# Optimization experiments

Hardware: AMD Instinct MI355X
Metric: run time of the kernel (lower is better)

Reference implementation:

```python
import jax, jax.numpy as jnp
import numpy as np

SEQ = 16384
D = 1024


def setup_inputs() -> dict:
    key = jax.random.key(0)
    k1, k2, k3, k4 = jax.random.split(key, 4)
    return {
        "G_M1": jax.random.normal(k1, (SEQ, D), dtype=jnp.float32),
        "G_M2": jax.random.normal(k2, (SEQ, D), dtype=jnp.float32),
        "wp1": jax.random.normal(k3, (1, D), dtype=jnp.float32),
        "wp2": jax.random.normal(k4, (1, D), dtype=jnp.float32),
    }


def reference(G_M1, G_M2, wp1, wp2):
    # Original: per-row tensordot(wp1, G_M1[i][:, None]) -> [1,1], concat along
    # axis 1 -> p1 of shape [1, SEQ]; same for p2; softmax over the seq axis.
    # This is exactly a single matvec per head followed by softmax.
    p1 = jnp.einsum("od,sd->os", wp1, G_M1)  # [1, SEQ]
    p2 = jnp.einsum("od,sd->os", wp2, G_M2)  # [1, SEQ]
    p1_pred = jax.nn.softmax(p1, axis=-1)
    p2_pred = jax.nn.softmax(p2, axis=-1)
    return (p1_pred, p2_pred)
```

## Files before the change

kernel.cpp:

```cpp
#include <hip/hip_runtime.h>
#include <hip/hip_bf16.h>
#include <math.h>

#define SEQ 16384
#define D   1024
#define NBLK_DOT 2048
#define WAVES_PER_BLK 4

__global__ __launch_bounds__(256) void dot_partial_kernel(
    const float* __restrict__ g1, const float* __restrict__ g2,
    const float* __restrict__ wp1, const float* __restrict__ wp2,
    float* __restrict__ logits,
    float* __restrict__ blk_m, float* __restrict__ blk_s) {
  const int lane = threadIdx.x & 63;
  const int wid  = threadIdx.x >> 6;
  const int w    = blockIdx.x * WAVES_PER_BLK + wid;
  const int r0   = w * 4;
  const bool head1 = (r0 >= SEQ);
  const float* g  = head1 ? g2 : g1;
  const float* wp = head1 ? wp2 : wp1;
  const int row0  = head1 ? (r0 - SEQ) : r0;

  const float4* wpv = (const float4*)wp;
  float4 wv[4];
#pragma unroll
  for (int k = 0; k < 4; ++k) wv[k] = wpv[lane + 64 * k];

  const float4* rv = (const float4*)(g + (size_t)row0 * D);
  float acc0 = 0.f, acc1 = 0.f, acc2 = 0.f, acc3 = 0.f;
#pragma unroll
  for (int k = 0; k < 4; ++k) {
    const int o = lane + 64 * k;
    float4 a0 = rv[o];
    float4 a1 = rv[o + 256];
    float4 a2 = rv[o + 512];
    float4 a3 = rv[o + 768];
    float4 wk = wv[k];
    acc0 = fmaf(a0.x, wk.x, fmaf(a0.y, wk.y, fmaf(a0.z, wk.z, fmaf(a0.w, wk.w, acc0))));
    acc1 = fmaf(a1.x, wk.x, fmaf(a1.y, wk.y, fmaf(a1.z, wk.z, fmaf(a1.w, wk.w, acc1))));
    acc2 = fmaf(a2.x, wk.x, fmaf(a2.y, wk.y, fmaf(a2.z, wk.z, fmaf(a2.w, wk.w, acc2))));
    acc3 = fmaf(a3.x, wk.x, fmaf(a3.y, wk.y, fmaf(a3.z, wk.z, fmaf(a3.w, wk.w, acc3))));
  }
#pragma unroll
  for (int off = 32; off > 0; off >>= 1) {
    acc0 += __shfl_xor(acc0, off, 64);
    acc1 += __shfl_xor(acc1, off, 64);
    acc2 += __shfl_xor(acc2, off, 64);
    acc3 += __shfl_xor(acc3, off, 64);
  }
  if (lane == 0) {
    *(float4*)(logits + r0) = make_float4(acc0, acc1, acc2, acc3);
  }

  float mw = fmaxf(fmaxf(acc0, acc1), fmaxf(acc2, acc3));
  float sw = __expf(acc0 - mw) + __expf(acc1 - mw) +
             __expf(acc2 - mw) + __expf(acc3 - mw);

  __shared__ float lm[WAVES_PER_BLK], ls[WAVES_PER_BLK];
  if (lane == 0) { lm[wid] = mw; ls[wid] = sw; }
  __syncthreads();
  if (threadIdx.x == 0) {
    float M = fmaxf(fmaxf(lm[0], lm[1]), fmaxf(lm[2], lm[3]));
    float S = ls[0] * __expf(lm[0] - M) + ls[1] * __expf(lm[1] - M) +
              ls[2] * __expf(lm[2] - M) + ls[3] * __expf(lm[3] - M);
    blk_m[blockIdx.x] = M;
    blk_s[blockIdx.x] = S;
  }
}

__global__ __launch_bounds__(1024) void stats_kernel(
    const float* __restrict__ blk_m, const float* __restrict__ blk_s,
    float* __restrict__ stats) {
  const int h    = blockIdx.x;
  const int tid  = threadIdx.x;
  const int lane = tid & 63;
  const int wid  = tid >> 6;

  float m = blk_m[h * 1024 + tid];
  float s = blk_s[h * 1024 + tid];

  __shared__ float sm[16], ssum[16];

  float mm = m;
#pragma unroll
  for (int off = 32; off > 0; off >>= 1)
    mm = fmaxf(mm, __shfl_xor(mm, off, 64));
  if (lane == 0) sm[wid] = mm;
  __syncthreads();
  float M = sm[0];
#pragma unroll
  for (int i = 1; i < 16; ++i) M = fmaxf(M, sm[i]);

  float c = s * __expf(m - M);
#pragma unroll
  for (int off = 32; off > 0; off >>= 1)
    c += __shfl_xor(c, off, 64);
  if (lane == 0) ssum[wid] = c;
  __syncthreads();
  if (tid == 0) {
    float S = 0.f;
#pragma unroll
    for (int i = 0; i < 16; ++i) S += ssum[i];
    stats[2 * h]     = M;
    stats[2 * h + 1] = 1.0f / S;
  }
}

__global__ __launch_bounds__(256) void normalize_kernel(
    const float4* __restrict__ logits4, const float* __restrict__ stats,
    float4* __restrict__ out4) {
  const int i = blockIdx.x * blockDim.x + threadIdx.x;
  const int h = i >> 12;
  const float M    = stats[2 * h];
  const float invS = stats[2 * h + 1];
  float4 v = logits4[i];
  float4 o;
  o.x = __expf(v.x - M) * invS;
  o.y = __expf(v.y - M) * invS;
  o.z = __expf(v.z - M) * invS;
  o.w = __expf(v.w - M) * invS;
  out4[i] = o;
}

extern "C" void kernel_launch(void* const* d_in, const int* in_sizes, int n_in,
                              void* d_out, int out_size, void* d_ws, size_t ws_size,
                              hipStream_t stream) {
  const float* g1  = (const float*)d_in[0];
  const float* g2  = (const float*)d_in[1];
  const float* wp1 = (const float*)d_in[2];
  const float* wp2 = (const float*)d_in[3];
  float* out = (float*)d_out;

  float* logits = (float*)d_ws;
  float* blk_m  = logits + 2 * SEQ;
  float* blk_s  = blk_m + NBLK_DOT;
  float* stats  = blk_s + NBLK_DOT;

  dot_partial_kernel<<<NBLK_DOT, 256, 0, stream>>>(g1, g2, wp1, wp2,
                                                   logits, blk_m, blk_s);
  stats_kernel<<<2, 1024, 0, stream>>>(blk_m, blk_s, stats);
  normalize_kernel<<<32, 256, 0, stream>>>((const float4*)logits, stats,
                                           (float4*)out);
}
```

Baseline: 153.3 us.

## Fuse softmax stats into normalize kernel, use nontemporal loads, two rows per wave

Merges the stats and normalize kernels into one finalize kernel, where each block redundantly reduces its head's per-block max/sum, which removes one launch. The dot kernel now handles two rows per wave across twice as many blocks. All row loads are issued up front as nontemporal loads so the streamed inputs do not pollute the cache. The cost is redundant reduction work in each of the 32 finalize blocks and a different load pattern in the bandwidth-bound dot kernel.

```diff
diff --git a/kernel.cpp b/kernel.cpp
--- a/kernel.cpp
+++ b/kernel.cpp
@@ -4,59 +4,71 @@
 
 #define SEQ 16384
 #define D   1024
-#define NBLK_DOT 2048
-#define WAVES_PER_BLK 4
+#define NBLK_DOT 4096
+#define ROWS_PER_WAVE 2
 
-__global__ __launch_bounds__(256) void dot_partial_kernel(
+typedef float floatx4 __attribute__((ext_vector_type(4)));
+
+__device__ __forceinline__ floatx4 nt_load4(const float* p) {
+  return __builtin_nontemporal_load((const floatx4*)p);
+}
+
+__global__ void dot_partial_kernel(
     const float* __restrict__ g1, const float* __restrict__ g2,
     const float* __restrict__ wp1, const float* __restrict__ wp2,
     float* __restrict__ logits,
     float* __restrict__ blk_m, float* __restrict__ blk_s) {
   const int lane = threadIdx.x & 63;
   const int wid  = threadIdx.x >> 6;
-  const int w    = blockIdx.x * WAVES_PER_BLK + wid;
-  const int r0   = w * 4;
-  const bool head1 = (r0 >= SEQ);
+  const int w    = blockIdx.x * 4 + wid;
+  const int r0   = w * ROWS_PER_WAVE;
+  const bool head1 = (blockIdx.x >= NBLK_DOT / 2);
   const float* g  = head1 ? g2 : g1;
   const float* wp = head1 ? wp2 : wp1;
   const int row0  = head1 ? (r0 - SEQ) : r0;
 
-  const float4* wpv = (const float4*)wp;
-  float4 wv[4];
+  floatx4 wv[4];
 #pragma unroll
-  for (int k = 0; k < 4; ++k) wv[k] = wpv[lane + 64 * k];
+  for (int k = 0; k < 4; ++k)
+    wv[k] = *((const floatx4*)wp + lane + 64 * k);
 
-  const float4* rv = (const float4*)(g + (size_t)row0 * D);
-  float acc0 = 0.f, acc1 = 0.f, acc2 = 0.f, acc3 = 0.f;
+  const float* row = g + (size_t)row0 * D;
+
+  floatx4 a0 = nt_load4(row + 4 * (lane));
+  floatx4 a1 = nt_load4(row + 4 * (lane + 64));
+  floatx4 a2 = nt_load4(row + 4 * (lane + 128));
+  floatx4 a3 = nt_load4(row + 4 * (lane + 192));
+  floatx4 b0 = nt_load4(row + D + 4 * (lane));
+  floatx4 b1 = nt_load4(row + D + 4 * (lane + 64));
+  floatx4 b2 = nt_load4(row + D + 4 * (lane + 128));
+  floatx4 b3 = nt_load4(row + D + 4 * (lane + 192));
+
+  float acc0 = 0.f, acc1 = 0.f;
 #pragma unroll
-  for (int k = 0; k < 4; ++k) {
-    const int o = lane + 64 * k;
-    float4 a0 = rv[o];
-    float4 a1 = rv[o + 256];
-    float4 a2 = rv[o + 512];
-    float4 a3 = rv[o + 768];
-    float4 wk = wv[k];
-    acc0 = fmaf(a0.x, wk.x, fmaf(a0.y, wk.y, fmaf(a0.z, wk.z, fmaf(a0.w, wk.w, acc0))));
-    acc1 = fmaf(a1.x, wk.x, fmaf(a1.y, wk.y, fmaf(a1.z, wk.z, fmaf(a1.w, wk.w, acc1))));
-    acc2 = fmaf(a2.x, wk.x, fmaf(a2.y, wk.y, fmaf(a2.z, wk.z, fmaf(a2.w, wk.w, acc2))));
-    acc3 = fmaf(a3.x, wk.x, fmaf(a3.y, wk.y, fmaf(a3.z, wk.z, fmaf(a3.w, wk.w, acc3))));
+  for (int e = 0; e < 4; ++e) {
+    acc0 = fmaf(a0[e], wv[0][e], acc0);
+    acc0 = fmaf(a1[e], wv[1][e], acc0);
+    acc0 = fmaf(a2[e], wv[2][e], acc0);
+    acc0 = fmaf(a3[e], wv[3][e], acc0);
+    acc1 = fmaf(b0[e], wv[0][e], acc1);
+    acc1 = fmaf(b1[e], wv[1][e], acc1);
+    acc1 = fmaf(b2[e], wv[2][e], acc1);
+    acc1 = fmaf(b3[e], wv[3][e], acc1);
   }
+
 #pragma unroll
   for (int off = 32; off > 0; off >>= 1) {
     acc0 += __shfl_xor(acc0, off, 64);
     acc1 += __shfl_xor(acc1, off, 64);
-    acc2 += __shfl_xor(acc2, off, 64);
-    acc3 += __shfl_xor(acc3, off, 64);
   }
   if (lane == 0) {
-    *(float4*)(logits + r0) = make_float4(acc0, acc1, acc2, acc3);
+    *(float2*)(logits + r0) = make_float2(acc0, acc1);
   }
 
-  float mw = fmaxf(fmaxf(acc0, acc1), fmaxf(acc2, acc3));
-  float sw = __expf(acc0 - mw) + __expf(acc1 - mw) +
-             __expf(acc2 - mw) + __expf(acc3 - mw);
+  float mw = fmaxf(acc0, acc1);
+  float sw = __expf(acc0 - mw) + __expf(acc1 - mw);
 
-  __shared__ float lm[WAVES_PER_BLK], ls[WAVES_PER_BLK];
+  __shared__ float lm[4], ls[4];
   if (lane == 0) { lm[wid] = mw; ls[wid] = sw; }
   __syncthreads();
   if (threadIdx.x == 0) {
@@ -68,57 +80,57 @@
   }
 }
 
-__global__ __launch_bounds__(1024) void stats_kernel(
+__global__ __launch_bounds__(256) void finalize_kernel(
     const float* __restrict__ blk_m, const float* __restrict__ blk_s,
-    float* __restrict__ stats) {
-  const int h    = blockIdx.x;
+    const float4* __restrict__ logits4, float4* __restrict__ out4) {
+  const int head = blockIdx.x >> 4;
   const int tid  = threadIdx.x;
   const int lane = tid & 63;
   const int wid  = tid >> 6;
 
-  float m = blk_m[h * 1024 + tid];
-  float s = blk_s[h * 1024 + tid];
-
-  __shared__ float sm[16], ssum[16];
-
-  float mm = m;
+  const float* pm = blk_m + head * (NBLK_DOT / 2) + tid * 8;
+  const float* ps = blk_s + head * (NBLK_DOT / 2) + tid * 8;
+  float M = -INFINITY, S = 0.f;
 #pragma unroll
-  for (int off = 32; off > 0; off >>= 1)
-    mm = fmaxf(mm, __shfl_xor(mm, off, 64));
-  if (lane == 0) sm[wid] = mm;
-  __syncthreads();
-  float M = sm[0];
+  for (int i = 0; i < 8; ++i) {
+    float m = pm[i], s = ps[i];
+    float nm = fmaxf(M, m);
+    S = S * __expf(M - nm) + s * __expf(m - nm);
+    M = nm;
+  }
 #pragma unroll
-  for (int i = 1; i < 16; ++i) M = fmaxf(M, sm[i]);
-
-  float c = s * __expf(m - M);
-#pragma unroll
-  for (int off = 32; off > 0; off >>= 1)
-    c += __shfl_xor(c, off, 64);
-  if (lane == 0) ssum[wid] = c;
+  for (int off = 32; off > 0; off >>= 1) {
+    float m2 = __shfl_xor(M, off, 64);
+    float s2 = __shfl_xor(S, off, 64);
+    float nm = fmaxf(M, m2);
+    S = S * __expf(M - nm) + s2 * __expf(m2 - nm);
+    M = nm;
+  }
+  __shared__ float sm[4], ss[4], fin[2];
+  if (lane == 0) { sm[wid] = M; ss[wid] = S; }
   __syncthreads();
   if (tid == 0) {
-    float S = 0.f;
+    float Mg = -INFINITY, Sg = 0.f;
 #pragma unroll
-    for (int i = 0; i < 16; ++i) S += ssum[i];
-    stats[2 * h]     = M;
-    stats[2 * h + 1] = 1.0f / S;
+    for (int i = 0; i < 4; ++i) {
+      float nm = fmaxf(Mg, sm[i]);
+      Sg = Sg * __expf(Mg - nm) + ss[i] * __expf(sm[i] - nm);
+      Mg = nm;
+    }
+    fin[0] = Mg;
+    fin[1] = 1.0f / Sg;
   }
-}
+  __syncthreads();
+  const float Mg   = fin[0];
+  const float invS = fin[1];
 
-__global__ __launch_bounds__(256) void normalize_kernel(
-    const float4* __restrict__ logits4, const float* __restrict__ stats,
-    float4* __restrict__ out4) {
-  const int i = blockIdx.x * blockDim.x + threadIdx.x;
-  const int h = i >> 12;
-  const float M    = stats[2 * h];
-  const float invS = stats[2 * h + 1];
+  const int i = head * 4096 + (blockIdx.x & 15) * 256 + tid;
   float4 v = logits4[i];
   float4 o;
-  o.x = __expf(v.x - M) * invS;
-  o.y = __expf(v.y - M) * invS;
-  o.z = __expf(v.z - M) * invS;
-  o.w = __expf(v.w - M) * invS;
+  o.x = __expf(v.x - Mg) * invS;
+  o.y = __expf(v.y - Mg) * invS;
+  o.z = __expf(v.z - Mg) * invS;
+  o.w = __expf(v.w - Mg) * invS;
   out4[i] = o;
 }
 
@@ -134,11 +146,9 @@
   float* logits = (float*)d_ws;
   float* blk_m  = logits + 2 * SEQ;
   float* blk_s  = blk_m + NBLK_DOT;
-  float* stats  = blk_s + NBLK_DOT;
 
   dot_partial_kernel<<<NBLK_DOT, 256, 0, stream>>>(g1, g2, wp1, wp2,
                                                    logits, blk_m, blk_s);
-  stats_kernel<<<2, 1024, 0, stream>>>(blk_m, blk_s, stats);
-  normalize_kernel<<<32, 256, 0, stream>>>((const float4*)logits, stats,
-                                           (float4*)out);
+  finalize_kernel<<<32, 256, 0, stream>>>(blk_m, blk_s,
+                                          (const float4*)logits, (float4*)out);
 }
```

Measured after the change: 141.9 us. 1.08x faster.
